# Kernel tuning notes

Measured on AMD Instinct MI355X. Metric: run time of the kernel, lower is better.

## Reference

```python
import jax, jax.numpy as jnp
import numpy as np

B, L, D, I, E, K = 2, 2048, 1024, 4096, 8, 2
LN_EPS = 1e-5


def _layernorm(x, g, b):
    m = jnp.mean(x, axis=-1, keepdims=True)
    v = jnp.mean(jnp.square(x - m), axis=-1, keepdims=True)
    return (x - m) * jax.lax.rsqrt(v + LN_EPS) * g + b


def setup_inputs() -> dict:
    key = jax.random.key(0)
    ks = jax.random.split(key, 4)
    return {
        "hidden_states": jax.random.normal(ks[0], (B, L, D), dtype=jnp.float32),
        "rn_g": jnp.ones((D,), jnp.float32),
        "rn_b": jnp.zeros((D,), jnp.float32),
        "router_w": jax.random.normal(ks[1], (E, D), jnp.float32) * 0.02,
        "router_b": jnp.zeros((E,), jnp.float32),
        "ln_g": jnp.ones((E, D), jnp.float32),
        "ln_b": jnp.zeros((E, D), jnp.float32),
        "w1": jax.random.normal(ks[2], (E, D, I), jnp.float32) * 0.02,
        "b1": jnp.zeros((E, I), jnp.float32),
        "w2": jax.random.normal(ks[3], (E, I, D), jnp.float32) * 0.02,
        "b2": jnp.zeros((E, D), jnp.float32),
    }


def reference(hidden_states, rn_g, rn_b, router_w, router_b, ln_g, ln_b, w1, b1, w2, b2):
    # Router (dropout is identity in eval mode)
    normed = _layernorm(hidden_states, rn_g, rn_b)
    logits = (jnp.einsum('bld,ed->ble', normed, router_w) + router_b).astype(jnp.float32)
    top_w, top_idx = jax.lax.top_k(logits, K)                    # [B,L,K]
    top_w = jax.nn.softmax(top_w, axis=-1).astype(hidden_states.dtype)
    # Per-token combine weight for each expert: sum over selected slots
    onehot = jax.nn.one_hot(top_idx, E, dtype=top_w.dtype)       # [B,L,K,E]
    combine = jnp.einsum('blke,blk->ble', onehot, top_w)         # [B,L,E]

    out = jnp.zeros_like(hidden_states)
    for e in range(E):  # fixed, small expert count
        h = _layernorm(hidden_states, ln_g[e], ln_b[e])
        h = jax.nn.gelu(jnp.einsum('bld,di->bli', h, w1[e]) + b1[e], approximate=False)
        h = jnp.einsum('bli,id->bld', h, w2[e]) + b2[e]
        out = out + combine[..., e:e + 1] * h
    return out
```

## Files before the change

kernel.cpp:

```cpp
#include <hip/hip_runtime.h>
#include <hip/hip_bf16.h>
#include <stdint.h>

#define T_TOK 4096
#define DDIM  1024
#define IDIM  4096
#define NEXP  8
#define GROWS (T_TOK*2 + 128)

typedef __attribute__((ext_vector_type(8))) short bfrag;
typedef __attribute__((ext_vector_type(4))) float f32x4;

__device__ __forceinline__ unsigned short f2bf(float x) {
    unsigned int u = __float_as_uint(x);
    unsigned int r = u + 0x7FFFu + ((u >> 16) & 1u);
    return (unsigned short)(r >> 16);
}
__device__ __forceinline__ float bf2f(unsigned short h) {
    return __uint_as_float(((unsigned int)h) << 16);
}

#define GLOAD16(gsrc, ldst)                                                     \
    __builtin_amdgcn_global_load_lds(                                           \
        (const __attribute__((address_space(1))) unsigned int*)(gsrc),          \
        (__attribute__((address_space(3))) unsigned int*)(ldst), 16, 0, 0)

__global__ __launch_bounds__(256) void router_kernel(
    const float* __restrict__ x,
    const float* __restrict__ rng, const float* __restrict__ rnb,
    const float* __restrict__ rw,  const float* __restrict__ rb,
    unsigned short* __restrict__ xhat,
    int* __restrict__ counts, int* __restrict__ tok_slot,
    float* __restrict__ wslot)
{
    const int t = blockIdx.x;
    const int tid = threadIdx.x;
    const int lane = tid & 63, wid = tid >> 6;

    float4 v = *(const float4*)(x + (size_t)t * DDIM + tid * 4);
    float s1 = v.x + v.y + v.z + v.w;
    float s2 = v.x*v.x + v.y*v.y + v.z*v.z + v.w*v.w;
    #pragma unroll
    for (int m = 32; m; m >>= 1) { s1 += __shfl_xor(s1, m, 64); s2 += __shfl_xor(s2, m, 64); }

    __shared__ float red[8];
    __shared__ float pl[4][8];
    __shared__ float bcast[2];
    if (lane == 0) { red[wid] = s1; red[wid + 4] = s2; }
    __syncthreads();
    if (tid == 0) {
        float S1 = red[0] + red[1] + red[2] + red[3];
        float S2 = red[4] + red[5] + red[6] + red[7];
        float mean = S1 * (1.f / 1024.f);
        float var  = S2 * (1.f / 1024.f) - mean * mean;
        bcast[0] = mean; bcast[1] = rsqrtf(var + 1e-5f);
    }
    __syncthreads();
    const float mean = bcast[0], rinv = bcast[1];

    float4 xh = { (v.x - mean) * rinv, (v.y - mean) * rinv,
                  (v.z - mean) * rinv, (v.w - mean) * rinv };
    ushort4 hx = { f2bf(xh.x), f2bf(xh.y), f2bf(xh.z), f2bf(xh.w) };
    *(ushort4*)(xhat + (size_t)t * DDIM + tid * 4) = hx;

    float4 g = *(const float4*)(rng + tid * 4);
    float4 b = *(const float4*)(rnb + tid * 4);
    float4 nm = { xh.x*g.x + b.x, xh.y*g.y + b.y, xh.z*g.z + b.z, xh.w*g.w + b.w };
    float p[8];
    #pragma unroll
    for (int e = 0; e < 8; e++) {
        float4 w = *(const float4*)(rw + e * DDIM + tid * 4);
        p[e] = nm.x*w.x + nm.y*w.y + nm.z*w.z + nm.w*w.w;
    }
    #pragma unroll
    for (int m = 32; m; m >>= 1) {
        #pragma unroll
        for (int e = 0; e < 8; e++) p[e] += __shfl_xor(p[e], m, 64);
    }
    if (lane == 0) {
        #pragma unroll
        for (int e = 0; e < 8; e++) pl[wid][e] = p[e];
    }
    __syncthreads();
    if (tid == 0) {
        float l[8];
        #pragma unroll
        for (int e = 0; e < 8; e++) l[e] = pl[0][e] + pl[1][e] + pl[2][e] + pl[3][e] + rb[e];
        int e0 = 0; float v0 = l[0];
        for (int e = 1; e < 8; e++) if (l[e] > v0) { v0 = l[e]; e0 = e; }
        int e1 = (e0 == 0) ? 1 : 0; float v1 = l[e1];
        for (int e = 0; e < 8; e++) if (e != e0 && l[e] > v1) { v1 = l[e]; e1 = e; }
        float ex = expf(v1 - v0);
        float w0 = 1.f / (1.f + ex);
        float w1 = ex * w0;
        int p0 = atomicAdd(&counts[e0], 1);
        tok_slot[e0 * T_TOK + p0] = (t << 1);
        int p1 = atomicAdd(&counts[e1], 1);
        tok_slot[e1 * T_TOK + p1] = (t << 1) | 1;
        wslot[t * 2]     = w0;
        wslot[t * 2 + 1] = w1;
    }
}

__global__ void prefix_kernel(const int* __restrict__ counts, int* __restrict__ offs)
{
    if (threadIdx.x == 0) {
        int a = 0;
        for (int e = 0; e < 8; e++) { offs[e] = a; a += counts[e]; }
    }
}

__global__ __launch_bounds__(256) void gather_kernel(
    const unsigned short* __restrict__ xhat,
    const float* __restrict__ lng, const float* __restrict__ lnb,
    const int* __restrict__ counts, const int* __restrict__ offs,
    const int* __restrict__ tok_slot,
    unsigned short* __restrict__ Agath, int* __restrict__ rowinfo)
{
    const int e = blockIdx.y, pos = blockIdx.x;
    if (pos >= counts[e]) return;
    const int grow = offs[e] + pos;
    const int info = tok_slot[e * T_TOK + pos];
    if (threadIdx.x == 0) rowinfo[grow] = info;
    const int t = info >> 1;
    const int d = threadIdx.x * 4;
    ushort4 hx = *(const ushort4*)(xhat + (size_t)t * DDIM + d);
    float4 g = *(const float4*)(lng + (size_t)e * DDIM + d);
    float4 b = *(const float4*)(lnb + (size_t)e * DDIM + d);
    ushort4 o = { f2bf(bf2f(hx.x) * g.x + b.x),
                  f2bf(bf2f(hx.y) * g.y + b.y),
                  f2bf(bf2f(hx.z) * g.z + b.z),
                  f2bf(bf2f(hx.w) * g.w + b.w) };
    *(ushort4*)(Agath + (size_t)grow * DDIM + d) = o;
}

__global__ __launch_bounds__(256) void transpose_kernel(
    const float* __restrict__ W, unsigned short* __restrict__ WT,
    int Kd, int Nd)
{
    const int e  = blockIdx.z;
    const int k0 = blockIdx.y * 64;
    const int n  = blockIdx.x * 256 + threadIdx.x;
    const float* src = W + (size_t)e * Kd * Nd + (size_t)k0 * Nd + n;
    unsigned short* dst = WT + ((size_t)e * Nd + n) * Kd + k0;
    unsigned short buf[64];
    #pragma unroll
    for (int j = 0; j < 64; j++)
        buf[j] = f2bf(src[(size_t)j * Nd]);
    #pragma unroll
    for (int c = 0; c < 8; c++)
        *(int4*)(dst + c * 8) = *(const int4*)(buf + c * 8);
}

template<int EPI>
__global__ __launch_bounds__(256) void gemm_kernel(
    const unsigned short* __restrict__ Asrc,
    const unsigned short* __restrict__ Bsrc,
    const float* __restrict__ bias,
    const int* __restrict__ counts,
    const int* __restrict__ offs,
    const int* __restrict__ rowinfo,
    const float* __restrict__ wslot,
    unsigned short* __restrict__ Hout,
    float* __restrict__ Out,
    int Kd, int Nd)
{
    const int e  = blockIdx.z;
    const int ne = counts[e];
    const int mt = blockIdx.y;
    if (mt * 128 >= ne) return;
    const int n0 = blockIdx.x * 128;
    const int growbase = offs[e] + mt * 128;
    const int tid  = threadIdx.x;
    const int lane = tid & 63;
    const int wm = (tid >> 7) & 1;
    const int wn = (tid >> 6) & 1;

    __shared__ unsigned short As[128 * 64];
    __shared__ unsigned short Bs[128 * 64];

    f32x4 acc[4][4];
    #pragma unroll
    for (int i = 0; i < 4; i++)
        #pragma unroll
        for (int j = 0; j < 4; j++)
            acc[i][j] = (f32x4){0.f, 0.f, 0.f, 0.f};

    const unsigned short* ap = Asrc + (size_t)(growbase + (tid >> 3)) * Kd + (tid & 7) * 8;
    const unsigned short* bp = Bsrc + ((size_t)e * Nd + n0 + (tid >> 3)) * Kd + (tid & 7) * 8;
    char* aldsw = (char*)As + (tid >> 6) * 1024;
    char* bldsw = (char*)Bs + (tid >> 6) * 1024;
    const size_t rowstep = (size_t)32 * Kd;

    for (int k0 = 0; k0 < Kd; k0 += 64) {
        __syncthreads();
        #pragma unroll
        for (int c = 0; c < 4; c++) {
            GLOAD16(ap + c * rowstep, aldsw + c * 4096);
            GLOAD16(bp + c * rowstep, bldsw + c * 4096);
        }
        ap += 64; bp += 64;
        __syncthreads();
        #pragma unroll
        for (int kk = 0; kk < 2; kk++) {
            bfrag av[4], bv[4];
            #pragma unroll
            for (int i = 0; i < 4; i++)
                av[i] = *(const bfrag*)((const char*)As +
                         (wm * 64 + i * 16 + (lane & 15)) * 128 + kk * 64 + ((lane >> 4) << 4));
            #pragma unroll
            for (int j = 0; j < 4; j++)
                bv[j] = *(const bfrag*)((const char*)Bs +
                         (wn * 64 + j * 16 + (lane & 15)) * 128 + kk * 64 + ((lane >> 4) << 4));
            #pragma unroll
            for (int i = 0; i < 4; i++)
                #pragma unroll
                for (int j = 0; j < 4; j++)
                    acc[i][j] = __builtin_amdgcn_mfma_f32_16x16x32_bf16(av[i], bv[j], acc[i][j], 0, 0, 0);
        }
    }

    const float* bg = bias + (size_t)e * Nd;
    #pragma unroll
    for (int i = 0; i < 4; i++) {
        #pragma unroll
        for (int r = 0; r < 4; r++) {
            int mrow = wm * 64 + i * 16 + ((lane >> 4) << 2) + r;
            int pos = mt * 128 + mrow;
            if (pos >= ne) continue;
            if constexpr (EPI == 0) {
                size_t rowoff = (size_t)(growbase + mrow) * Nd;
                #pragma unroll
                for (int j = 0; j < 4; j++) {
                    int col = n0 + wn * 64 + j * 16 + (lane & 15);
                    float y = acc[i][j][r] + bg[col];
                    float gl = 0.5f * y * (1.f + erff(y * 0.70710678118654752f));
                    Hout[rowoff + col] = f2bf(gl);
                }
            } else {
                int info = rowinfo[growbase + mrow];
                float wg = wslot[info];
                float* op = Out + (size_t)(info >> 1) * Nd;
                #pragma unroll
                for (int j = 0; j < 4; j++) {
                    int col = n0 + wn * 64 + j * 16 + (lane & 15);
                    float y = acc[i][j][r] + bg[col];
                    atomicAdd(op + col, wg * y);
                }
            }
        }
    }
}

extern "C" void kernel_launch(void* const* d_in, const int* in_sizes, int n_in,
                              void* d_out, int out_size, void* d_ws, size_t ws_size,
                              hipStream_t stream)
{
    (void)in_sizes; (void)n_in;
    const float* hidden   = (const float*)d_in[0];
    const float* rn_g     = (const float*)d_in[1];
    const float* rn_b     = (const float*)d_in[2];
    const float* router_w = (const float*)d_in[3];
    const float* router_b = (const float*)d_in[4];
    const float* ln_g     = (const float*)d_in[5];
    const float* ln_b     = (const float*)d_in[6];
    const float* w1       = (const float*)d_in[7];
    const float* b1       = (const float*)d_in[8];
    const float* w2       = (const float*)d_in[9];
    const float* b2       = (const float*)d_in[10];
    float* out = (float*)d_out;

    char* ws = (char*)d_ws;
    unsigned short* xhat   = (unsigned short*)ws;
    unsigned short* Agath  = (unsigned short*)(ws + 8388608);
    unsigned short* H      = (unsigned short*)(ws + 25427968);
    unsigned short* WT     = (unsigned short*)(ws + 93585408);
    int*   counts   = (int*)(ws + 160694272);
    int*   offs     = (int*)(ws + 160694304);
    int*   tok_slot = (int*)(ws + 160694336);
    int*   rowinfo  = (int*)(ws + 160825408);
    float* wslot    = (float*)(ws + 160858688);
    if (ws_size < 160891456) return;

    hipMemsetAsync(counts, 0, 64, stream);
    hipMemsetAsync(d_out, 0, (size_t)out_size * sizeof(float), stream);

    transpose_kernel<<<dim3(IDIM / 256, DDIM / 64, NEXP), 256, 0, stream>>>(w1, WT, DDIM, IDIM);
    router_kernel<<<T_TOK, 256, 0, stream>>>(hidden, rn_g, rn_b, router_w, router_b,
                                             xhat, counts, tok_slot, wslot);
    prefix_kernel<<<1, 64, 0, stream>>>(counts, offs);
    gather_kernel<<<dim3(T_TOK, NEXP), 256, 0, stream>>>(xhat, ln_g, ln_b, counts, offs,
                                                         tok_slot, Agath, rowinfo);
    gemm_kernel<0><<<dim3(IDIM / 128, 32, NEXP), 256, 0, stream>>>(
        Agath, WT, b1, counts, offs, rowinfo, wslot, H, nullptr, DDIM, IDIM);
    transpose_kernel<<<dim3(DDIM / 256, IDIM / 64, NEXP), 256, 0, stream>>>(w2, WT, IDIM, DDIM);
    gemm_kernel<1><<<dim3(DDIM / 128, 32, NEXP), 256, 0, stream>>>(
        H, WT, b2, counts, offs, rowinfo, wslot, nullptr, out, IDIM, DDIM);
}
```

Baseline: 622.7 us.

## Double-buffer LDS tiles in grouped expert GEMM to overlap loads with MFMA

Turns the single shared-memory A/B tile in the grouped expert GEMM into two buffers. The next K-slice is issued via global_load_lds into the alternate buffer before the MFMA work on the current buffer, leaving one barrier per iteration instead of two. The aim is to hide global-to-LDS latency behind compute. LDS use doubles to 64KB per block, which may reduce occupancy.

```diff
diff --git a/kernel.cpp b/kernel.cpp
--- a/kernel.cpp
+++ b/kernel.cpp
@@ -176,8 +176,8 @@
     const int wm = (tid >> 7) & 1;
     const int wn = (tid >> 6) & 1;
 
-    __shared__ unsigned short As[128 * 64];
-    __shared__ unsigned short Bs[128 * 64];
+    __shared__ unsigned short As[2][128 * 64];
+    __shared__ unsigned short Bs[2][128 * 64];
 
     f32x4 acc[4][4];
     #pragma unroll
@@ -188,29 +188,42 @@
 
     const unsigned short* ap = Asrc + (size_t)(growbase + (tid >> 3)) * Kd + (tid & 7) * 8;
     const unsigned short* bp = Bsrc + ((size_t)e * Nd + n0 + (tid >> 3)) * Kd + (tid & 7) * 8;
-    char* aldsw = (char*)As + (tid >> 6) * 1024;
-    char* bldsw = (char*)Bs + (tid >> 6) * 1024;
     const size_t rowstep = (size_t)32 * Kd;
-
-    for (int k0 = 0; k0 < Kd; k0 += 64) {
-        __syncthreads();
-        #pragma unroll
-        for (int c = 0; c < 4; c++) {
-            GLOAD16(ap + c * rowstep, aldsw + c * 4096);
-            GLOAD16(bp + c * rowstep, bldsw + c * 4096);
+    char* const aw = (char*)As + (tid >> 6) * 1024;
+    char* const bw = (char*)Bs + (tid >> 6) * 1024;
+
+    #pragma unroll
+    for (int c = 0; c < 4; c++) {
+        GLOAD16(ap + c * rowstep, aw + c * 4096);
+        GLOAD16(bp + c * rowstep, bw + c * 4096);
+    }
+    ap += 64; bp += 64;
+    __syncthreads();
+
+    const int nt = Kd >> 6;
+    int cur = 0;
+    for (int t = 0; t < nt; ++t) {
+        if (t + 1 < nt) {
+            const int nxt = (cur ^ 1) * 16384;
+            #pragma unroll
+            for (int c = 0; c < 4; c++) {
+                GLOAD16(ap + c * rowstep, aw + nxt + c * 4096);
+                GLOAD16(bp + c * rowstep, bw + nxt + c * 4096);
+            }
+            ap += 64; bp += 64;
         }
-        ap += 64; bp += 64;
-        __syncthreads();
+        const char* Ab = (const char*)As + cur * 16384;
+        const char* Bb = (const char*)Bs + cur * 16384;
         #pragma unroll
         for (int kk = 0; kk < 2; kk++) {
             bfrag av[4], bv[4];
             #pragma unroll
             for (int i = 0; i < 4; i++)
-                av[i] = *(const bfrag*)((const char*)As +
+                av[i] = *(const bfrag*)(Ab +
                          (wm * 64 + i * 16 + (lane & 15)) * 128 + kk * 64 + ((lane >> 4) << 4));
             #pragma unroll
             for (int j = 0; j < 4; j++)
-                bv[j] = *(const bfrag*)((const char*)Bs +
+                bv[j] = *(const bfrag*)(Bb +
                          (wn * 64 + j * 16 + (lane & 15)) * 128 + kk * 64 + ((lane >> 4) << 4));
             #pragma unroll
             for (int i = 0; i < 4; i++)
@@ -218,6 +231,8 @@
                 for (int j = 0; j < 4; j++)
                     acc[i][j] = __builtin_amdgcn_mfma_f32_16x16x32_bf16(av[i], bv[j], acc[i][j], 0, 0, 0);
         }
+        __syncthreads();
+        cur ^= 1;
     }
 
     const float* bg = bias + (size_t)e * Nd;
```

New measurement: 614.8 us. Within noise of the previous version (-1.3%).

## Triple-buffer grouped GEMM with 256-row tiles, 512 threads and 1D expert-interleaved grid

Applied to the files above, without the earlier changes.

Restructures the grouped expert GEMM to use 256x128 tiles across 8 waves, with a three-slot LDS ring buffer. Global-to-LDS loads for tile t+2 are issued in two halves interleaved with the MFMA work, synchronised by explicit waitcnt and barriers. It also raises MFMA priority with setprio, uses a fragment-native LDS layout, and flattens the grid so blocks interleave across experts. The goal is to hide load latency and cut per-iteration barrier stalls. The trade-offs are larger LDS use (144 KB per block) and possibly lower occupancy, plus more padding waste for experts with small token counts.

```diff
diff --git a/kernel.cpp b/kernel.cpp
--- a/kernel.cpp
+++ b/kernel.cpp
@@ -6,7 +6,7 @@
 #define DDIM  1024
 #define IDIM  4096
 #define NEXP  8
-#define GROWS (T_TOK*2 + 128)
+#define GROWS (T_TOK*2 + 256)
 
 typedef __attribute__((ext_vector_type(8))) short bfrag;
 typedef __attribute__((ext_vector_type(4))) float f32x4;
@@ -153,7 +153,7 @@
 }
 
 template<int EPI>
-__global__ __launch_bounds__(256) void gemm_kernel(
+__global__ __launch_bounds__(512, 2) void gemm_kernel(
     const unsigned short* __restrict__ Asrc,
     const unsigned short* __restrict__ Bsrc,
     const float* __restrict__ bias,
@@ -165,19 +165,24 @@
     float* __restrict__ Out,
     int Kd, int Nd)
 {
-    const int e  = blockIdx.z;
+    const int b  = blockIdx.x;
+    const int e  = b & 7;
+    const int r  = b >> 3;
+    const int mt = r & 15;
+    const int nt = r >> 4;
     const int ne = counts[e];
-    const int mt = blockIdx.y;
-    if (mt * 128 >= ne) return;
-    const int n0 = blockIdx.x * 128;
-    const int growbase = offs[e] + mt * 128;
+    if (mt * 256 >= ne) return;
+    const int n0 = nt * 128;
+    const int growbase = offs[e] + mt * 256;
+
     const int tid  = threadIdx.x;
     const int lane = tid & 63;
-    const int wm = (tid >> 7) & 1;
-    const int wn = (tid >> 6) & 1;
-
-    __shared__ unsigned short As[128 * 64];
-    __shared__ unsigned short Bs[128 * 64];
+    const int wid  = tid >> 6;
+    const int wm   = wid >> 1;
+    const int wn   = wid & 1;
+
+    __shared__ unsigned short S[3 * 24576];
+    char* const Sb = (char*)S;
 
     f32x4 acc[4][4];
     #pragma unroll
@@ -186,54 +191,95 @@
         for (int j = 0; j < 4; j++)
             acc[i][j] = (f32x4){0.f, 0.f, 0.f, 0.f};
 
-    const unsigned short* ap = Asrc + (size_t)(growbase + (tid >> 3)) * Kd + (tid & 7) * 8;
-    const unsigned short* bp = Bsrc + ((size_t)e * Nd + n0 + (tid >> 3)) * Kd + (tid & 7) * 8;
-    char* aldsw = (char*)As + (tid >> 6) * 1024;
-    char* bldsw = (char*)Bs + (tid >> 6) * 1024;
-    const size_t rowstep = (size_t)32 * Kd;
-
-    for (int k0 = 0; k0 < Kd; k0 += 64) {
-        __syncthreads();
-        #pragma unroll
-        for (int c = 0; c < 4; c++) {
-            GLOAD16(ap + c * rowstep, aldsw + c * 4096);
-            GLOAD16(bp + c * rowstep, bldsw + c * 4096);
-        }
-        ap += 64; bp += 64;
-        __syncthreads();
-        #pragma unroll
-        for (int kk = 0; kk < 2; kk++) {
+    const unsigned short* Abase = Asrc + (size_t)growbase * Kd;
+    const unsigned short* Bbase = Bsrc + ((size_t)e * Nd + n0) * Kd;
+    const int laneoff = (lane & 15) * Kd + (lane >> 4) * 8;
+
+    #define STAGE_A(q, m) do {                                                    \
+        const int c_ = wid + 8 * (m);                                             \
+        GLOAD16(Abase + (size_t)((c_ >> 1) * 16) * Kd + laneoff                    \
+                      + (q) * 64 + (c_ & 1) * 32,                                  \
+                Sb + ((q) % 3) * 49152 + c_ * 1024);                               \
+    } while (0)
+    #define STAGE_B(q, m) do {                                                    \
+        const int c_ = wid + 8 * (m);                                             \
+        GLOAD16(Bbase + (size_t)((c_ >> 1) * 16) * Kd + laneoff                    \
+                      + (q) * 64 + (c_ & 1) * 32,                                  \
+                Sb + ((q) % 3) * 49152 + 32768 + c_ * 1024);                       \
+    } while (0)
+
+    const int ntile = Kd >> 6;
+
+    STAGE_A(0, 0); STAGE_A(0, 1); STAGE_A(0, 2); STAGE_A(0, 3);
+    STAGE_B(0, 0); STAGE_B(0, 1);
+    STAGE_A(1, 0); STAGE_A(1, 1); STAGE_A(1, 2); STAGE_A(1, 3);
+    STAGE_B(1, 0); STAGE_B(1, 1);
+
+    for (int t = 0; t < ntile; ++t) {
+        const char* Aslot = Sb + (t % 3) * 49152;
+        const char* Bslot = Aslot + 32768;
+
+        asm volatile("s_waitcnt lgkmcnt(0)" ::: "memory");
+        if (t < ntile - 1) asm volatile("s_waitcnt vmcnt(6)" ::: "memory");
+        else               asm volatile("s_waitcnt vmcnt(0)" ::: "memory");
+        __builtin_amdgcn_s_barrier();
+
+        const bool pf = (t + 2 < ntile);
+
+        if (pf) { STAGE_A(t + 2, 0); STAGE_A(t + 2, 1); STAGE_A(t + 2, 2); }
+        {
             bfrag av[4], bv[4];
             #pragma unroll
             for (int i = 0; i < 4; i++)
-                av[i] = *(const bfrag*)((const char*)As +
-                         (wm * 64 + i * 16 + (lane & 15)) * 128 + kk * 64 + ((lane >> 4) << 4));
+                av[i] = *(const bfrag*)(Aslot + ((wm * 4 + i) * 2 + 0) * 1024 + lane * 16);
             #pragma unroll
             for (int j = 0; j < 4; j++)
-                bv[j] = *(const bfrag*)((const char*)Bs +
-                         (wn * 64 + j * 16 + (lane & 15)) * 128 + kk * 64 + ((lane >> 4) << 4));
+                bv[j] = *(const bfrag*)(Bslot + ((wn * 4 + j) * 2 + 0) * 1024 + lane * 16);
+            __builtin_amdgcn_s_setprio(1);
             #pragma unroll
             for (int i = 0; i < 4; i++)
                 #pragma unroll
                 for (int j = 0; j < 4; j++)
                     acc[i][j] = __builtin_amdgcn_mfma_f32_16x16x32_bf16(av[i], bv[j], acc[i][j], 0, 0, 0);
+            __builtin_amdgcn_s_setprio(0);
         }
-    }
+        __builtin_amdgcn_s_barrier();
+
+        if (pf) { STAGE_A(t + 2, 3); STAGE_B(t + 2, 0); STAGE_B(t + 2, 1); }
+        {
+            bfrag av[4], bv[4];
+            #pragma unroll
+            for (int i = 0; i < 4; i++)
+                av[i] = *(const bfrag*)(Aslot + ((wm * 4 + i) * 2 + 1) * 1024 + lane * 16);
+            #pragma unroll
+            for (int j = 0; j < 4; j++)
+                bv[j] = *(const bfrag*)(Bslot + ((wn * 4 + j) * 2 + 1) * 1024 + lane * 16);
+            __builtin_amdgcn_s_setprio(1);
+            #pragma unroll
+            for (int i = 0; i < 4; i++)
+                #pragma unroll
+                for (int j = 0; j < 4; j++)
+                    acc[i][j] = __builtin_amdgcn_mfma_f32_16x16x32_bf16(av[i], bv[j], acc[i][j], 0, 0, 0);
+            __builtin_amdgcn_s_setprio(0);
+        }
+    }
+    #undef STAGE_A
+    #undef STAGE_B
 
     const float* bg = bias + (size_t)e * Nd;
     #pragma unroll
     for (int i = 0; i < 4; i++) {
         #pragma unroll
-        for (int r = 0; r < 4; r++) {
-            int mrow = wm * 64 + i * 16 + ((lane >> 4) << 2) + r;
-            int pos = mt * 128 + mrow;
+        for (int rr = 0; rr < 4; rr++) {
+            int mrow = wm * 64 + i * 16 + ((lane >> 4) << 2) + rr;
+            int pos = mt * 256 + mrow;
             if (pos >= ne) continue;
             if constexpr (EPI == 0) {
                 size_t rowoff = (size_t)(growbase + mrow) * Nd;
                 #pragma unroll
                 for (int j = 0; j < 4; j++) {
                     int col = n0 + wn * 64 + j * 16 + (lane & 15);
-                    float y = acc[i][j][r] + bg[col];
+                    float y = acc[i][j][rr] + bg[col];
                     float gl = 0.5f * y * (1.f + erff(y * 0.70710678118654752f));
                     Hout[rowoff + col] = f2bf(gl);
                 }
@@ -244,7 +290,7 @@
                 #pragma unroll
                 for (int j = 0; j < 4; j++) {
                     int col = n0 + wn * 64 + j * 16 + (lane & 15);
-                    float y = acc[i][j][r] + bg[col];
+                    float y = acc[i][j][rr] + bg[col];
                     atomicAdd(op + col, wg * y);
                 }
             }
@@ -273,14 +319,14 @@
     char* ws = (char*)d_ws;
     unsigned short* xhat   = (unsigned short*)ws;
     unsigned short* Agath  = (unsigned short*)(ws + 8388608);
-    unsigned short* H      = (unsigned short*)(ws + 25427968);
-    unsigned short* WT     = (unsigned short*)(ws + 93585408);
-    int*   counts   = (int*)(ws + 160694272);
-    int*   offs     = (int*)(ws + 160694304);
-    int*   tok_slot = (int*)(ws + 160694336);
-    int*   rowinfo  = (int*)(ws + 160825408);
-    float* wslot    = (float*)(ws + 160858688);
-    if (ws_size < 160891456) return;
+    unsigned short* H      = (unsigned short*)(ws + 25690112);
+    unsigned short* WT     = (unsigned short*)(ws + 94896128);
+    int*   counts   = (int*)(ws + 162004992);
+    int*   offs     = (int*)(ws + 162005024);
+    int*   tok_slot = (int*)(ws + 162005056);
+    int*   rowinfo  = (int*)(ws + 162136128);
+    float* wslot    = (float*)(ws + 162169920);
+    if (ws_size < 162202688) return;
 
     hipMemsetAsync(counts, 0, 64, stream);
     hipMemsetAsync(d_out, 0, (size_t)out_size * sizeof(float), stream);
@@ -291,9 +337,9 @@
     prefix_kernel<<<1, 64, 0, stream>>>(counts, offs);
     gather_kernel<<<dim3(T_TOK, NEXP), 256, 0, stream>>>(xhat, ln_g, ln_b, counts, offs,
                                                          tok_slot, Agath, rowinfo);
-    gemm_kernel<0><<<dim3(IDIM / 128, 32, NEXP), 256, 0, stream>>>(
+    gemm_kernel<0><<<dim3(8 * 16 * (IDIM / 128)), 512, 0, stream>>>(
         Agath, WT, b1, counts, offs, rowinfo, wslot, H, nullptr, DDIM, IDIM);
     transpose_kernel<<<dim3(DDIM / 256, IDIM / 64, NEXP), 256, 0, stream>>>(w2, WT, IDIM, DDIM);
-    gemm_kernel<1><<<dim3(DDIM / 128, 32, NEXP), 256, 0, stream>>>(
+    gemm_kernel<1><<<dim3(8 * 16 * (DDIM / 128)), 512, 0, stream>>>(
         H, WT, b2, counts, offs, rowinfo, wslot, nullptr, out, IDIM, DDIM);
 }
```

Result: slower. 751.2 us (+20.6%).

## Double-buffer grouped GEMM with 8-wave blocks and strided M-tile loop

Applied to the files above, without the earlier changes.

Rewrites the grouped expert GEMM to use 512-thread blocks and a double-buffered LDS pipeline. The next K-slice is prefetched with global_load_lds while MFMAs run on the current one, synchronised with explicit vmcnt waits and raw barriers. The LDS layout now matches the MFMA fragment order, so fragment reads are contiguous per lane. A flattened 1D grid assigns each block a fixed expert and N tile and strides over M tiles, replacing the 3D grid that launched many empty blocks. The risks are load imbalance across experts and register pressure from the new launch bounds.

```diff
diff --git a/kernel.cpp b/kernel.cpp
--- a/kernel.cpp
+++ b/kernel.cpp
@@ -6,7 +6,7 @@
 #define DDIM  1024
 #define IDIM  4096
 #define NEXP  8
-#define GROWS (T_TOK*2 + 128)
+#define GROWS (T_TOK*2 + 256)
 
 typedef __attribute__((ext_vector_type(8))) short bfrag;
 typedef __attribute__((ext_vector_type(4))) float f32x4;
@@ -153,7 +153,7 @@
 }
 
 template<int EPI>
-__global__ __launch_bounds__(256) void gemm_kernel(
+__global__ __launch_bounds__(512, 4) void gemm_kernel(
     const unsigned short* __restrict__ Asrc,
     const unsigned short* __restrict__ Bsrc,
     const float* __restrict__ bias,
@@ -165,87 +165,109 @@
     float* __restrict__ Out,
     int Kd, int Nd)
 {
-    const int e  = blockIdx.z;
-    const int ne = counts[e];
-    const int mt = blockIdx.y;
-    if (mt * 128 >= ne) return;
-    const int n0 = blockIdx.x * 128;
-    const int growbase = offs[e] + mt * 128;
+    const int b   = blockIdx.x;
+    const int e   = b & 7;
+    const int r   = b >> 3;
+    const int mt0 = r & 7;
+    const int nt  = r >> 3;
+    const int ne  = counts[e];
+    const int n0  = nt * 128;
+
     const int tid  = threadIdx.x;
     const int lane = tid & 63;
-    const int wm = (tid >> 7) & 1;
-    const int wn = (tid >> 6) & 1;
-
-    __shared__ unsigned short As[128 * 64];
-    __shared__ unsigned short Bs[128 * 64];
-
-    f32x4 acc[4][4];
-    #pragma unroll
-    for (int i = 0; i < 4; i++)
-        #pragma unroll
-        for (int j = 0; j < 4; j++)
-            acc[i][j] = (f32x4){0.f, 0.f, 0.f, 0.f};
-
-    const unsigned short* ap = Asrc + (size_t)(growbase + (tid >> 3)) * Kd + (tid & 7) * 8;
-    const unsigned short* bp = Bsrc + ((size_t)e * Nd + n0 + (tid >> 3)) * Kd + (tid & 7) * 8;
-    char* aldsw = (char*)As + (tid >> 6) * 1024;
-    char* bldsw = (char*)Bs + (tid >> 6) * 1024;
-    const size_t rowstep = (size_t)32 * Kd;
-
-    for (int k0 = 0; k0 < Kd; k0 += 64) {
-        __syncthreads();
-        #pragma unroll
-        for (int c = 0; c < 4; c++) {
-            GLOAD16(ap + c * rowstep, aldsw + c * 4096);
-            GLOAD16(bp + c * rowstep, bldsw + c * 4096);
-        }
-        ap += 64; bp += 64;
-        __syncthreads();
-        #pragma unroll
-        for (int kk = 0; kk < 2; kk++) {
-            bfrag av[4], bv[4];
-            #pragma unroll
-            for (int i = 0; i < 4; i++)
-                av[i] = *(const bfrag*)((const char*)As +
-                         (wm * 64 + i * 16 + (lane & 15)) * 128 + kk * 64 + ((lane >> 4) << 4));
+    const int wid  = tid >> 6;
+    const int wm   = wid >> 1;
+    const int wn   = wid & 1;
+
+    __shared__ unsigned short S[2 * 16384];
+    char* const Sb = (char*)S;
+
+    char* const aw = Sb + wid * 2048;
+    char* const bw = Sb + 16384 + wid * 2048;
+    const unsigned short* const bbase =
+        Bsrc + ((size_t)e * Nd + n0 + wid * 16 + (lane & 15)) * Kd + (lane >> 4) * 8;
+    const int nt_k = Kd >> 6;
+    const float* bg = bias + (size_t)e * Nd;
+
+    for (int mt = mt0; mt * 128 < ne; mt += 8) {
+        const int growbase = offs[e] + mt * 128;
+        const unsigned short* ap =
+            Asrc + (size_t)(growbase + wid * 16 + (lane & 15)) * Kd + (lane >> 4) * 8;
+        const unsigned short* bp = bbase;
+
+        f32x4 acc[2][4];
+        #pragma unroll
+        for (int i = 0; i < 2; i++)
             #pragma unroll
             for (int j = 0; j < 4; j++)
-                bv[j] = *(const bfrag*)((const char*)Bs +
-                         (wn * 64 + j * 16 + (lane & 15)) * 128 + kk * 64 + ((lane >> 4) << 4));
+                acc[i][j] = (f32x4){0.f, 0.f, 0.f, 0.f};
+
+        GLOAD16(ap, aw);      GLOAD16(ap + 32, aw + 1024);
+        GLOAD16(bp, bw);      GLOAD16(bp + 32, bw + 1024);
+        ap += 64; bp += 64;
+
+        for (int t = 0; t < nt_k; ++t) {
+            const int s = (t & 1) * 32768;
+            if (t + 1 < nt_k) {
+                const int s2 = ((t + 1) & 1) * 32768;
+                GLOAD16(ap, aw + s2);      GLOAD16(ap + 32, aw + s2 + 1024);
+                GLOAD16(bp, bw + s2);      GLOAD16(bp + 32, bw + s2 + 1024);
+                ap += 64; bp += 64;
+                asm volatile("s_waitcnt vmcnt(4)" ::: "memory");
+            } else {
+                asm volatile("s_waitcnt vmcnt(0)" ::: "memory");
+            }
+            __builtin_amdgcn_s_barrier();
+
+            const char* As_ = Sb + s;
+            const char* Bs_ = Sb + s + 16384;
             #pragma unroll
-            for (int i = 0; i < 4; i++)
+            for (int kk = 0; kk < 2; kk++) {
+                bfrag av[2], bv[4];
+                #pragma unroll
+                for (int i = 0; i < 2; i++)
+                    av[i] = *(const bfrag*)(As_ + ((wm * 2 + i) * 2 + kk) * 1024 + lane * 16);
                 #pragma unroll
                 for (int j = 0; j < 4; j++)
-                    acc[i][j] = __builtin_amdgcn_mfma_f32_16x16x32_bf16(av[i], bv[j], acc[i][j], 0, 0, 0);
+                    bv[j] = *(const bfrag*)(Bs_ + ((wn * 4 + j) * 2 + kk) * 1024 + lane * 16);
+                __builtin_amdgcn_s_setprio(1);
+                #pragma unroll
+                for (int i = 0; i < 2; i++)
+                    #pragma unroll
+                    for (int j = 0; j < 4; j++)
+                        acc[i][j] = __builtin_amdgcn_mfma_f32_16x16x32_bf16(av[i], bv[j], acc[i][j], 0, 0, 0);
+                __builtin_amdgcn_s_setprio(0);
+            }
+            asm volatile("s_waitcnt lgkmcnt(0)" ::: "memory");
+            __builtin_amdgcn_s_barrier();
         }
-    }
-
-    const float* bg = bias + (size_t)e * Nd;
-    #pragma unroll
-    for (int i = 0; i < 4; i++) {
-        #pragma unroll
-        for (int r = 0; r < 4; r++) {
-            int mrow = wm * 64 + i * 16 + ((lane >> 4) << 2) + r;
-            int pos = mt * 128 + mrow;
-            if (pos >= ne) continue;
-            if constexpr (EPI == 0) {
-                size_t rowoff = (size_t)(growbase + mrow) * Nd;
-                #pragma unroll
-                for (int j = 0; j < 4; j++) {
-                    int col = n0 + wn * 64 + j * 16 + (lane & 15);
-                    float y = acc[i][j][r] + bg[col];
-                    float gl = 0.5f * y * (1.f + erff(y * 0.70710678118654752f));
-                    Hout[rowoff + col] = f2bf(gl);
-                }
-            } else {
-                int info = rowinfo[growbase + mrow];
-                float wg = wslot[info];
-                float* op = Out + (size_t)(info >> 1) * Nd;
-                #pragma unroll
-                for (int j = 0; j < 4; j++) {
-                    int col = n0 + wn * 64 + j * 16 + (lane & 15);
-                    float y = acc[i][j][r] + bg[col];
-                    atomicAdd(op + col, wg * y);
+
+        #pragma unroll
+        for (int i = 0; i < 2; i++) {
+            #pragma unroll
+            for (int rr = 0; rr < 4; rr++) {
+                int mrow = wm * 32 + i * 16 + ((lane >> 4) << 2) + rr;
+                int pos = mt * 128 + mrow;
+                if (pos >= ne) continue;
+                if constexpr (EPI == 0) {
+                    size_t rowoff = (size_t)(growbase + mrow) * Nd;
+                    #pragma unroll
+                    for (int j = 0; j < 4; j++) {
+                        int col = n0 + wn * 64 + j * 16 + (lane & 15);
+                        float y = acc[i][j][rr] + bg[col];
+                        float gl = 0.5f * y * (1.f + erff(y * 0.70710678118654752f));
+                        Hout[rowoff + col] = f2bf(gl);
+                    }
+                } else {
+                    int info = rowinfo[growbase + mrow];
+                    float wg = wslot[info];
+                    float* op = Out + (size_t)(info >> 1) * Nd;
+                    #pragma unroll
+                    for (int j = 0; j < 4; j++) {
+                        int col = n0 + wn * 64 + j * 16 + (lane & 15);
+                        float y = acc[i][j][rr] + bg[col];
+                        atomicAdd(op + col, wg * y);
+                    }
                 }
             }
         }
@@ -273,14 +295,14 @@
     char* ws = (char*)d_ws;
     unsigned short* xhat   = (unsigned short*)ws;
     unsigned short* Agath  = (unsigned short*)(ws + 8388608);
-    unsigned short* H      = (unsigned short*)(ws + 25427968);
-    unsigned short* WT     = (unsigned short*)(ws + 93585408);
-    int*   counts   = (int*)(ws + 160694272);
-    int*   offs     = (int*)(ws + 160694304);
-    int*   tok_slot = (int*)(ws + 160694336);
-    int*   rowinfo  = (int*)(ws + 160825408);
-    float* wslot    = (float*)(ws + 160858688);
-    if (ws_size < 160891456) return;
+    unsigned short* H      = (unsigned short*)(ws + 25690112);
+    unsigned short* WT     = (unsigned short*)(ws + 94896128);
+    int*   counts   = (int*)(ws + 162004992);
+    int*   offs     = (int*)(ws + 162005024);
+    int*   tok_slot = (int*)(ws + 162005056);
+    int*   rowinfo  = (int*)(ws + 162136128);
+    float* wslot    = (float*)(ws + 162169920);
+    if (ws_size < 162202688) return;
 
     hipMemsetAsync(counts, 0, 64, stream);
     hipMemsetAsync(d_out, 0, (size_t)out_size * sizeof(float), stream);
@@ -291,9 +313,9 @@
     prefix_kernel<<<1, 64, 0, stream>>>(counts, offs);
     gather_kernel<<<dim3(T_TOK, NEXP), 256, 0, stream>>>(xhat, ln_g, ln_b, counts, offs,
                                                          tok_slot, Agath, rowinfo);
-    gemm_kernel<0><<<dim3(IDIM / 128, 32, NEXP), 256, 0, stream>>>(
+    gemm_kernel<0><<<dim3(8 * 8 * (IDIM / 128)), 512, 0, stream>>>(
         Agath, WT, b1, counts, offs, rowinfo, wslot, H, nullptr, DDIM, IDIM);
     transpose_kernel<<<dim3(DDIM / 256, IDIM / 64, NEXP), 256, 0, stream>>>(w2, WT, IDIM, DDIM);
-    gemm_kernel<1><<<dim3(DDIM / 128, 32, NEXP), 256, 0, stream>>>(
+    gemm_kernel<1><<<dim3(8 * 8 * (DDIM / 128)), 512, 0, stream>>>(
         H, WT, b2, counts, offs, rowinfo, wslot, nullptr, out, IDIM, DDIM);
 }
```

After: 703.6 us. +13.0%, slower.
